# Kernel optimization log

Measured on AMD Instinct MI355X. Metric: run time of the kernel, lower is better.

The kernel has to match this reference:

```python
import jax, jax.numpy as jnp
import numpy as np

H = 128

def _gru_cell(x, h, w_ih, w_hh, b_ih, b_hh):
    # PyTorch GRUCell semantics; w_* are [3H, H], gate order r, z, n.
    gi = x @ w_ih.T + b_ih
    gh = h @ w_hh.T + b_hh
    ir, iz, in_ = jnp.split(gi, 3, axis=-1)
    hr, hz, hn = jnp.split(gh, 3, axis=-1)
    r = jax.nn.sigmoid(ir + hr)
    z = jax.nn.sigmoid(iz + hz)
    n = jnp.tanh(in_ + r * hn)
    return (1.0 - z) * n + z * h


def setup_inputs() -> dict:
    key = jax.random.key(0)
    ks = jax.random.split(key, 24)
    s = 0.05
    d = {}
    d["weapon_features"] = jax.random.normal(ks[0], (4, 8, 64, 4), jnp.float32)
    d["target_features"] = jax.random.normal(ks[1], (4, 8, 64, 4), jnp.float32)
    d["edge_features"] = jax.random.uniform(ks[2], (4, 8, 64, 64, 1), jnp.float32)
    # projections (torch Linear convention: weight [out, in])
    d["wp_w"] = jax.random.normal(ks[3], (H, 4), jnp.float32) * s
    d["wp_b"] = jnp.zeros((H,), jnp.float32)
    d["tp_w"] = jax.random.normal(ks[4], (H, 4), jnp.float32) * s
    d["tp_b"] = jnp.zeros((H,), jnp.float32)
    d["ep_w"] = jax.random.normal(ks[5], (H, 1), jnp.float32) * s
    d["ep_b"] = jnp.zeros((H,), jnp.float32)
    # message / edge-update linears [H, 3H]
    d["eu_w"] = jax.random.normal(ks[6], (H, 3 * H), jnp.float32) * s
    d["eu_b"] = jnp.zeros((H,), jnp.float32)
    d["wm_w"] = jax.random.normal(ks[7], (H, 3 * H), jnp.float32) * s
    d["wm_b"] = jnp.zeros((H,), jnp.float32)
    d["tm_w"] = jax.random.normal(ks[8], (H, 3 * H), jnp.float32) * s
    d["tm_b"] = jnp.zeros((H,), jnp.float32)
    # GRU cells
    d["gru_w_ih_w"] = jax.random.normal(ks[9], (3 * H, H), jnp.float32) * s
    d["gru_w_hh_w"] = jax.random.normal(ks[10], (3 * H, H), jnp.float32) * s
    d["gru_b_ih_w"] = jnp.zeros((3 * H,), jnp.float32)
    d["gru_b_hh_w"] = jnp.zeros((3 * H,), jnp.float32)
    d["gru_w_ih_t"] = jax.random.normal(ks[11], (3 * H, H), jnp.float32) * s
    d["gru_w_hh_t"] = jax.random.normal(ks[12], (3 * H, H), jnp.float32) * s
    d["gru_b_ih_t"] = jnp.zeros((3 * H,), jnp.float32)
    d["gru_b_hh_t"] = jnp.zeros((3 * H,), jnp.float32)
    return d


def reference(weapon_features, target_features, edge_features,
              wp_w, wp_b, tp_w, tp_b, ep_w, ep_b,
              eu_w, eu_b, wm_w, wm_b, tm_w, tm_b,
              gru_w_ih_w, gru_w_hh_w, gru_b_ih_w, gru_b_hh_w,
              gru_w_ih_t, gru_w_hh_t, gru_b_ih_t, gru_b_hh_t):
    B, P, W = weapon_features.shape[:3]
    T = target_features.shape[2]
    h = wp_w.shape[0]

    weapon_h = weapon_features @ wp_w.T + wp_b          # [B,P,W,H]
    target_h = target_features @ tp_w.T + tp_b          # [B,P,T,H]
    edge_h = edge_features @ ep_w.T + ep_b              # [B,P,W,T,H]

    # edge_update(cat([w_exp, t_exp, edge_h])) == sum of three slice-linears,
    # broadcast-added; avoids materializing the [B,P,W,T,3H] concat.
    ea, eb, ec = eu_w[:, :h], eu_w[:, h:2 * h], eu_w[:, 2 * h:]
    edge_pre = ((weapon_h @ ea.T)[:, :, :, None, :]
                + (target_h @ eb.T)[:, :, None, :, :]
                + edge_h @ ec.T + eu_b)
    edge_h_new = jnp.tanh(edge_pre)                     # [B,P,W,T,H]

    # weapon_msg(cat([w_exp, t_exp, edge_h_new])).sum(dim=3)
    wa, wb, wc = wm_w[:, :h], wm_w[:, h:2 * h], wm_w[:, 2 * h:]
    weapon_msgs = (T * (weapon_h @ wa.T)
                   + (target_h.sum(axis=2) @ wb.T)[:, :, None, :]
                   + edge_h_new.sum(axis=3) @ wc.T
                   + T * wm_b)                          # [B,P,W,H]

    # target_msg(cat([t_exp, w_exp, edge_h_new])).sum(dim=2)
    ta, tb, tc = tm_w[:, :h], tm_w[:, h:2 * h], tm_w[:, 2 * h:]
    target_msgs = (W * (target_h @ ta.T)
                   + (weapon_h.sum(axis=2) @ tb.T)[:, :, None, :]
                   + edge_h_new.sum(axis=2) @ tc.T
                   + W * tm_b)                          # [B,P,T,H]

    weapon_h_new = _gru_cell(weapon_msgs.reshape(-1, h), weapon_h.reshape(-1, h),
                             gru_w_ih_w, gru_w_hh_w, gru_b_ih_w, gru_b_hh_w)
    weapon_h_new = weapon_h_new.reshape(B, P, W, h)

    target_h_new = _gru_cell(target_msgs.reshape(-1, h), target_h.reshape(-1, h),
                             gru_w_ih_t, gru_w_hh_t, gru_b_ih_t, gru_b_hh_t)
    target_h_new = target_h_new.reshape(B, P, T, h)

    return weapon_h_new, target_h_new, edge_h_new
```

## Files before the change

### kernel.cpp

```cpp
#include <hip/hip_runtime.h>

#define DEV __device__ __forceinline__

constexpr int H  = 128;
constexpr int BP = 32;
constexpr int NR = 2048;

constexpr int WH_OFF    = 0;
constexpr int TH_OFF    = WH_OFF + NR*H;
constexpr int WHS_OFF   = TH_OFF + NR*H;
constexpr int THS_OFF   = WHS_OFF + BP*H;
constexpr int V1_OFF    = THS_OFF + BP*H;
constexpr int C0_OFF    = V1_OFF + H;
constexpr int WT1_OFF   = C0_OFF + H;
constexpr int WT2_OFF   = WT1_OFF + 128*640;
constexpr int WCT_OFF   = WT2_OFF + 128*640;
constexpr int TCT_OFF   = WCT_OFF + 128*128;
constexpr int WIHWT_OFF = TCT_OFF + 128*128;
constexpr int WIHTT_OFF = WIHWT_OFF + 128*384;
constexpr int WBT_OFF   = WIHTT_OFF + 128*384;
constexpr int TBT_OFF   = WBT_OFF + 128*128;
constexpr int OUT1_OFF  = TBT_OFF + 128*128;
constexpr int OUT2_OFF  = OUT1_OFF + NR*640;
constexpr int ESW_OFF   = OUT2_OFF + NR*640;
constexpr int ESTP_OFF  = ESW_OFF + NR*H;
constexpr int MSGW_OFF  = ESTP_OFF + 8*NR*H;
constexpr int MSGT_OFF  = MSGW_OFF + NR*H;
constexpr int GIW_OFF   = MSGT_OFF + NR*H;
constexpr int GIT_OFF   = GIW_OFF + NR*384;
constexpr int WBV_OFF   = GIT_OFF + NR*384;
constexpr int TBV_OFF   = WBV_OFF + BP*H;

DEV float fast_tanh(float x) {
  float e = __builtin_amdgcn_exp2f(x * 2.8853900817779268f);
  return fmaf(-2.0f, __builtin_amdgcn_rcpf(e + 1.0f), 1.0f);
}
DEV float fast_sigmoid(float x) {
  float e = __builtin_amdgcn_exp2f(x * -1.4426950408889634f);
  return __builtin_amdgcn_rcpf(1.0f + e);
}

__global__ __launch_bounds__(256) void ka_prep(
    const float* __restrict__ wf, const float* __restrict__ tf,
    const float* __restrict__ wp_w, const float* __restrict__ wp_b,
    const float* __restrict__ tp_w, const float* __restrict__ tp_b,
    const float* __restrict__ eu_w, const float* __restrict__ wm_w,
    const float* __restrict__ tm_w,
    const float* __restrict__ whh_w, const float* __restrict__ whh_t,
    const float* __restrict__ wih_w, const float* __restrict__ wih_t,
    const float* __restrict__ ep_w, const float* __restrict__ ep_b,
    const float* __restrict__ eu_b,
    float* __restrict__ ws)
{
  int bid = blockIdx.x, tid = threadIdx.x;
  if (bid < 2048) {
    int gid = bid*256 + tid;
    int m = gid >> 7;
    int j = gid & 127;
    int side = m >> 11;
    int n = m & 2047;
    const float* F  = side ? tf : wf;
    const float* Pw = side ? tp_w : wp_w;
    const float* Pb = side ? tp_b : wp_b;
    float4 x  = *(const float4*)&F[n*4];
    float4 wv = *(const float4*)&Pw[j*4];
    float v = x.x*wv.x + x.y*wv.y + x.z*wv.z + x.w*wv.w + Pb[j];
    ws[(side ? TH_OFF : WH_OFF) + n*H + j] = v;
  } else if (bid == 2048) {
    __shared__ float fs[2][32][4];
    {
      int side = tid >> 7, r = tid & 127;
      int bp = r >> 2, c = r & 3;
      const float* F = side ? tf : wf;
      float s = 0.f;
      #pragma unroll 8
      for (int w = 0; w < 64; ++w) s += F[bp*256 + w*4 + c];
      fs[side][bp][c] = s;
    }
    __syncthreads();
    {
      int side = tid >> 7, j = tid & 127;
      const float* Pw = side ? tp_w : wp_w;
      const float* Pb = side ? tp_b : wp_b;
      float4 wv = *(const float4*)&Pw[j*4];
      float pb = Pb[j] * 64.f;
      float* dst = ws + (side ? THS_OFF : WHS_OFF) + j;
      #pragma unroll 4
      for (int bp = 0; bp < 32; ++bp) {
        float4 f = *(const float4*)&fs[side][bp][0];
        dst[bp*128] = f.x*wv.x + f.y*wv.y + f.z*wv.z + f.w*wv.w + pb;
      }
    }
    if (tid < 128) {
      int j = tid;
      float s1 = 0.f, s0 = 0.f;
      for (int k = 0; k < 128; ++k) {
        float ec = eu_w[j*384 + 256 + k];
        s1 = fmaf(ec, ep_w[k], s1);
        s0 = fmaf(ec, ep_b[k], s0);
      }
      ws[V1_OFF + j] = s1;
      ws[C0_OFF + j] = s0 + eu_b[j];
    }
  } else {
    __shared__ float T[128*133];
    int tt = bid - 2049;
    const float* src; int rs = 384, co = 0, row0 = 0, dsto, ldd, j0;
    switch (tt) {
      case 0:  src=eu_w;  dsto=WT1_OFF; ldd=640; j0=0;   break;
      case 1:  src=wm_w;  dsto=WT1_OFF; ldd=640; j0=128; break;
      case 2: case 3: case 4:
        src=whh_w; rs=128; row0=(tt-2)*128; dsto=WT1_OFF; ldd=640; j0=256+(tt-2)*128; break;
      case 5:  src=eu_w;  co=128; dsto=WT2_OFF; ldd=640; j0=0; break;
      case 6:  src=tm_w;  dsto=WT2_OFF; ldd=640; j0=128; break;
      case 7: case 8: case 9:
        src=whh_t; rs=128; row0=(tt-7)*128; dsto=WT2_OFF; ldd=640; j0=256+(tt-7)*128; break;
      case 10: src=wm_w; co=256; dsto=WCT_OFF; ldd=128; j0=0; break;
      case 11: src=tm_w; co=256; dsto=TCT_OFF; ldd=128; j0=0; break;
      case 12: src=wm_w; co=128; dsto=WBT_OFF; ldd=128; j0=0; break;
      case 13: src=tm_w; co=128; dsto=TBT_OFF; ldd=128; j0=0; break;
      case 14: case 15: case 16:
        src=wih_w; rs=128; row0=(tt-14)*128; dsto=WIHWT_OFF; ldd=384; j0=(tt-14)*128; break;
      default:
        src=wih_t; rs=128; row0=(tt-17)*128; dsto=WIHTT_OFF; ldd=384; j0=(tt-17)*128; break;
    }
    #pragma unroll
    for (int q = 0; q < 16; ++q) {
      int idx = q*1024 + tid*4;
      int r = idx >> 7, c = idx & 127;
      float4 v = *(const float4*)&src[(row0 + r)*rs + co + c];
      float* t = &T[r*133 + c];
      t[0]=v.x; t[1]=v.y; t[2]=v.z; t[3]=v.w;
    }
    __syncthreads();
    float* dst = ws + dsto;
    #pragma unroll
    for (int q = 0; q < 64; ++q) {
      int idx = q*256 + tid;
      int k = idx >> 7, j = idx & 127;
      dst[k*ldd + j0 + j] = T[j*133 + k];
    }
  }
}

#define FMA4(A, s, Wv) do { A.x = fmaf(s, Wv.x, A.x); A.y = fmaf(s, Wv.y, A.y); \
                            A.z = fmaf(s, Wv.z, A.z); A.w = fmaf(s, Wv.w, A.w); } while (0)

DEV void stage_x32(float* Xs, const float* __restrict__ X, int row0, int tid) {
  const float* src = X + row0*128;
  #pragma unroll
  for (int q = 0; q < 4; ++q) {
    int idx = q*1024 + tid*4;
    *(float4*)&Xs[idx] = *(const float4*)&src[idx];
  }
}

DEV void stage_x64(float* Xs, const float* __restrict__ X, int row0, int tid) {
  const float* src = X + row0*128;
  #pragma unroll
  for (int q = 0; q < 8; ++q) {
    int idx = q*1024 + tid*4;
    *(float4*)&Xs[idx] = *(const float4*)&src[idx];
  }
}

DEV void stage_x_sum8(float* Xs, const float* __restrict__ base, int row0, int tid) {
  #pragma unroll
  for (int q = 0; q < 4; ++q) {
    int idx = q*1024 + tid*4;
    float4 s = *(const float4*)&base[row0*128 + idx];
    #pragma unroll
    for (int wt = 1; wt < 8; ++wt) {
      float4 v = *(const float4*)&base[wt*(NR*H) + row0*128 + idx];
      s.x += v.x; s.y += v.y; s.z += v.z; s.w += v.w;
    }
    *(float4*)&Xs[idx] = s;
  }
}

DEV void gemm_core32(const float* __restrict__ Wt, int ldw, int j0,
                     const float* Xs, float* Ws, int tid, float4 acc[4])
{
  const int tc = tid & 31, tr = tid >> 5;
  const int jj = tc*4, r0 = tr*4;
  #pragma unroll
  for (int i = 0; i < 4; ++i) acc[i] = make_float4(0.f, 0.f, 0.f, 0.f);
  for (int kc = 0; kc < 128; kc += 32) {
    __syncthreads();
    #pragma unroll
    for (int q = 0; q < 4; ++q) {
      int idx = q*1024 + tid*4;
      int kk = idx >> 7, j = idx & 127;
      *(float4*)&Ws[idx] = *(const float4*)&Wt[(kc+kk)*ldw + j0 + j];
    }
    __syncthreads();
    #pragma unroll
    for (int kk = 0; kk < 32; kk += 4) {
      float4 w0 = *(const float4*)&Ws[(kk+0)*128 + jj];
      float4 w1 = *(const float4*)&Ws[(kk+1)*128 + jj];
      float4 w2 = *(const float4*)&Ws[(kk+2)*128 + jj];
      float4 w3 = *(const float4*)&Ws[(kk+3)*128 + jj];
      #pragma unroll
      for (int rr = 0; rr < 4; ++rr) {
        float4 xq = *(const float4*)&Xs[(r0+rr)*128 + kc + kk];
        FMA4(acc[rr], xq.x, w0);
        FMA4(acc[rr], xq.y, w1);
        FMA4(acc[rr], xq.z, w2);
        FMA4(acc[rr], xq.w, w3);
      }
    }
  }
}

DEV void gemm_core64(const float* __restrict__ Wt, int ldw, int j0,
                     const float* Xs, float* Ws, int tid, float4 acc[8])
{
  const int tc = tid & 31, tr = tid >> 5;
  const int jj = tc*4, r0 = tr*8;
  #pragma unroll
  for (int i = 0; i < 8; ++i) acc[i] = make_float4(0.f, 0.f, 0.f, 0.f);
  for (int kc = 0; kc < 128; kc += 32) {
    __syncthreads();
    #pragma unroll
    for (int q = 0; q < 4; ++q) {
      int idx = q*1024 + tid*4;
      int kk = idx >> 7, j = idx & 127;
      *(float4*)&Ws[idx] = *(const float4*)&Wt[(kc+kk)*ldw + j0 + j];
    }
    __syncthreads();
    #pragma unroll
    for (int kk = 0; kk < 32; kk += 4) {
      float4 w0 = *(const float4*)&Ws[(kk+0)*128 + jj];
      float4 w1 = *(const float4*)&Ws[(kk+1)*128 + jj];
      float4 w2 = *(const float4*)&Ws[(kk+2)*128 + jj];
      float4 w3 = *(const float4*)&Ws[(kk+3)*128 + jj];
      #pragma unroll
      for (int rr = 0; rr < 8; ++rr) {
        float4 xq = *(const float4*)&Xs[(r0+rr)*128 + kc + kk];
        FMA4(acc[rr], xq.x, w0);
        FMA4(acc[rr], xq.y, w1);
        FMA4(acc[rr], xq.z, w2);
        FMA4(acc[rr], xq.w, w3);
      }
    }
  }
}

__global__ __launch_bounds__(256) void kb_gemm1(float* __restrict__ ws)
{
  __shared__ float Xs[64*128];
  __shared__ float Wsh[32*128];
  int bid = blockIdx.x, tid = threadIdx.x;
  const int tc = tid & 31, tr = tid >> 5;
  const int jj = tc*4;
  if (bid < 320) {
    int side = bid >= 160;
    int b2 = bid - (side ? 160 : 0);
    int rt = b2 & 31, ct = b2 >> 5;
    int row0 = rt*64;
    stage_x64(Xs, ws + (side ? TH_OFF : WH_OFF), row0, tid);
    float4 acc[8];
    gemm_core64(ws + (side ? WT2_OFF : WT1_OFF), 640, ct*128, Xs, Wsh, tid, acc);
    float* C = ws + (side ? OUT2_OFF : OUT1_OFF);
    const int r0 = tr*8;
    #pragma unroll
    for (int rr = 0; rr < 8; ++rr)
      *(float4*)&C[(row0+r0+rr)*640 + ct*128 + jj] = acc[rr];
  } else {
    int which = bid - 320;
    stage_x32(Xs, ws + (which ? WHS_OFF : THS_OFF), 0, tid);
    float4 acc[4];
    gemm_core32(ws + (which ? TBT_OFF : WBT_OFF), 128, 0, Xs, Wsh, tid, acc);
    float* C = ws + (which ? TBV_OFF : WBV_OFF);
    const int r0 = tr*4;
    #pragma unroll
    for (int rr = 0; rr < 4; ++rr)
      *(float4*)&C[(r0+rr)*128 + jj] = acc[rr];
  }
}

__global__ __launch_bounds__(256) void kc_edge(
    const float* __restrict__ ef, float* __restrict__ ws, float* __restrict__ out)
{
  __shared__ float Bs[64*128];
  __shared__ float e_lds[8*64];
  __shared__ float red[2][8][128];
  int bid = blockIdx.x, tid = threadIdx.x;
  int bp = bid >> 3, wq = bid & 7;
  int j = tid & 127, tsel = tid >> 7;
  float v1j = ws[V1_OFF + j], c0j = ws[C0_OFF + j];
  {
    const float* o2 = ws + OUT2_OFF + bp*64*640;
    #pragma unroll
    for (int q = 0; q < 8; ++q) {
      int idx = q*256 + tid;
      int t = idx >> 5, jq = (idx & 31)*4;
      *(float4*)&Bs[t*128 + jq] = *(const float4*)&o2[t*640 + jq];
    }
  }
  if (tid < 128) {
    int w = tid >> 4, t4 = (tid & 15)*4;
    *(float4*)&e_lds[w*64 + t4] = *(const float4*)&ef[bp*4096 + (wq*8 + w)*64 + t4];
  }
  float a_reg[8];
  #pragma unroll
  for (int w = 0; w < 8; ++w)
    a_reg[w] = ws[OUT1_OFF + (bp*64 + wq*8 + w)*640 + j];
  __syncthreads();
  float tsum[8] = {0,0,0,0,0,0,0,0};
  float* edst = out + 524288 + (bp*64 + wq*8)*8192 + j;
  float* pdst = ws + ESTP_OFF + wq*(NR*H) + bp*64*128 + j;
  for (int i = 0; i < 32; ++i) {
    int t = 2*i + tsel;
    float base = Bs[t*128 + j] + c0j;
    float wsum = 0.f;
    #pragma unroll
    for (int w = 0; w < 8; ++w) {
      float ev = e_lds[w*64 + t];
      float pre = a_reg[w] + fmaf(ev, v1j, base);
      float hv = fast_tanh(pre);
      __builtin_nontemporal_store(hv, &edst[w*8192 + t*128]);
      tsum[w] += hv;
      wsum += hv;
    }
    pdst[t*128] = wsum;
  }
  #pragma unroll
  for (int w = 0; w < 8; ++w) red[tsel][w][j] = tsum[w];
  __syncthreads();
  if (tsel == 0) {
    #pragma unroll
    for (int w = 0; w < 8; ++w)
      ws[ESW_OFF + (bp*64 + wq*8 + w)*128 + j] = red[0][w][j] + red[1][w][j];
  }
}

__global__ __launch_bounds__(256) void kd_gemm2(
    float* __restrict__ ws, const float* __restrict__ wm_b, const float* __restrict__ tm_b)
{
  __shared__ float Xs[32*128];
  __shared__ float Wsh[32*128];
  int bid = blockIdx.x, tid = threadIdx.x;
  int side = bid >> 6, rt = bid & 63;
  int row0 = rt*32;
  const int tc = tid & 31, tr = tid >> 5;
  const int jj = tc*4, r0 = tr*4;
  if (side == 0) stage_x32(Xs, ws + ESW_OFF, row0, tid);
  else           stage_x_sum8(Xs, ws + ESTP_OFF, row0, tid);
  float4 acc[4];
  gemm_core32(ws + (side ? TCT_OFF : WCT_OFF), 128, 0, Xs, Wsh, tid, acc);
  const float* OUTx = ws + (side ? OUT2_OFF : OUT1_OFF);
  const float* BV   = ws + (side ? TBV_OFF : WBV_OFF);
  const float* mb   = side ? tm_b : wm_b;
  float* MSG        = ws + (side ? MSGT_OFF : MSGW_OFF);
  float4 b4 = *(const float4*)&mb[jj];
  #pragma unroll
  for (int rr = 0; rr < 4; ++rr) {
    int n = row0 + r0 + rr;
    float4 wa4 = *(const float4*)&OUTx[n*640 + 128 + jj];
    float4 bv4 = *(const float4*)&BV[(n >> 6)*128 + jj];
    float4 r;
    r.x = acc[rr].x + 64.f*(wa4.x + b4.x) + bv4.x;
    r.y = acc[rr].y + 64.f*(wa4.y + b4.y) + bv4.y;
    r.z = acc[rr].z + 64.f*(wa4.z + b4.z) + bv4.z;
    r.w = acc[rr].w + 64.f*(wa4.w + b4.w) + bv4.w;
    *(float4*)&MSG[n*128 + jj] = r;
  }
}

__global__ __launch_bounds__(256) void ke_gemm3(float* __restrict__ ws)
{
  __shared__ float Xs[32*128];
  __shared__ float Wsh[32*128];
  int bid = blockIdx.x, tid = threadIdx.x;
  int side = bid >= 192;
  int b2 = bid - (side ? 192 : 0);
  int rt = b2 & 63, ct = b2 >> 6;
  int row0 = rt*32;
  const int tc = tid & 31, tr = tid >> 5;
  const int jj = tc*4, r0 = tr*4;
  stage_x32(Xs, ws + (side ? MSGT_OFF : MSGW_OFF), row0, tid);
  float4 acc[4];
  gemm_core32(ws + (side ? WIHTT_OFF : WIHWT_OFF), 384, ct*128, Xs, Wsh, tid, acc);
  float* C = ws + (side ? GIT_OFF : GIW_OFF);
  #pragma unroll
  for (int rr = 0; rr < 4; ++rr)
    *(float4*)&C[(row0+r0+rr)*384 + ct*128 + jj] = acc[rr];
}

__global__ __launch_bounds__(256) void kf_gru(
    const float* __restrict__ ws, float* __restrict__ out,
    const float* __restrict__ bih_w, const float* __restrict__ bhh_w,
    const float* __restrict__ bih_t, const float* __restrict__ bhh_t)
{
  int gid = blockIdx.x*256 + threadIdx.x;
  int jj = (gid & 31)*4;
  int n  = (gid >> 5) & 2047;
  int side = gid >> 16;
  const float* GI = ws + (side ? GIT_OFF : GIW_OFF) + n*384;
  const float* GH = ws + (side ? OUT2_OFF : OUT1_OFF) + n*640 + 256;
  const float* Hv = ws + (side ? TH_OFF : WH_OFF) + n*128;
  const float* bi = side ? bih_t : bih_w;
  const float* bh = side ? bhh_t : bhh_w;
  float4 gir = *(const float4*)&GI[jj];
  float4 giz = *(const float4*)&GI[128 + jj];
  float4 gin = *(const float4*)&GI[256 + jj];
  float4 ghr = *(const float4*)&GH[jj];
  float4 ghz = *(const float4*)&GH[128 + jj];
  float4 ghn = *(const float4*)&GH[256 + jj];
  float4 bir = *(const float4*)&bi[jj];
  float4 biz = *(const float4*)&bi[128 + jj];
  float4 bin = *(const float4*)&bi[256 + jj];
  float4 bhr = *(const float4*)&bh[jj];
  float4 bhz = *(const float4*)&bh[128 + jj];
  float4 bhn = *(const float4*)&bh[256 + jj];
  float4 h4  = *(const float4*)&Hv[jj];
  float4 o;
  #define GRU1(c) do { \
    float r = fast_sigmoid(gir.c + bir.c + ghr.c + bhr.c); \
    float z = fast_sigmoid(giz.c + biz.c + ghz.c + bhz.c); \
    float nn = fast_tanh(gin.c + bin.c + r*(ghn.c + bhn.c)); \
    o.c = (1.f - z)*nn + z*h4.c; } while (0)
  GRU1(x); GRU1(y); GRU1(z); GRU1(w);
  #undef GRU1
  __builtin_nontemporal_store(o.x, &out[side*262144 + n*128 + jj + 0]);
  __builtin_nontemporal_store(o.y, &out[side*262144 + n*128 + jj + 1]);
  __builtin_nontemporal_store(o.z, &out[side*262144 + n*128 + jj + 2]);
  __builtin_nontemporal_store(o.w, &out[side*262144 + n*128 + jj + 3]);
}

extern "C" void kernel_launch(void* const* d_in, const int* in_sizes, int n_in,
                              void* d_out, int out_size, void* d_ws, size_t ws_size,
                              hipStream_t stream)
{
  const float* wf    = (const float*)d_in[0];
  const float* tf    = (const float*)d_in[1];
  const float* ef    = (const float*)d_in[2];
  const float* wp_w  = (const float*)d_in[3];
  const float* wp_b  = (const float*)d_in[4];
  const float* tp_w  = (const float*)d_in[5];
  const float* tp_b  = (const float*)d_in[6];
  const float* ep_w  = (const float*)d_in[7];
  const float* ep_b  = (const float*)d_in[8];
  const float* eu_w  = (const float*)d_in[9];
  const float* eu_b  = (const float*)d_in[10];
  const float* wm_w  = (const float*)d_in[11];
  const float* wm_b  = (const float*)d_in[12];
  const float* tm_w  = (const float*)d_in[13];
  const float* tm_b  = (const float*)d_in[14];
  const float* wih_w = (const float*)d_in[15];
  const float* whh_w = (const float*)d_in[16];
  const float* bih_w = (const float*)d_in[17];
  const float* bhh_w = (const float*)d_in[18];
  const float* wih_t = (const float*)d_in[19];
  const float* whh_t = (const float*)d_in[20];
  const float* bih_t = (const float*)d_in[21];
  const float* bhh_t = (const float*)d_in[22];
  float* ws  = (float*)d_ws;
  float* out = (float*)d_out;

  hipLaunchKernelGGL(ka_prep, dim3(2069), dim3(256), 0, stream,
                     wf, tf, wp_w, wp_b, tp_w, tp_b, eu_w, wm_w, tm_w,
                     whh_w, whh_t, wih_w, wih_t, ep_w, ep_b, eu_b, ws);
  hipLaunchKernelGGL(kb_gemm1, dim3(322),  dim3(256), 0, stream, ws);
  hipLaunchKernelGGL(kc_edge,  dim3(256),  dim3(256), 0, stream, ef, ws, out);
  hipLaunchKernelGGL(kd_gemm2, dim3(128),  dim3(256), 0, stream, ws, wm_b, tm_b);
  hipLaunchKernelGGL(ke_gemm3, dim3(384),  dim3(256), 0, stream, ws);
  hipLaunchKernelGGL(kf_gru,   dim3(512),  dim3(256), 0, stream, ws, out,
                     bih_w, bhh_w, bih_t, bhh_t);
}
```

Baseline: 186.6 us.

## Fuse projections into GEMM1 and merge message, input-gate GEMM and GRU kernels

The node feature projections and per-batch sums move out of the prep kernel and are computed in shared memory inside the first GEMM. That GEMM also writes the projected hidden states for later use. The message GEMM, the GRU input GEMM and the GRU elementwise step are merged into one kernel working on 16-row tiles, so the MSG and GI intermediates never go through global memory. This cuts the launch count from six to four and removes several global round trips. In exchange, the fused kernel has smaller tiles and repeats the weight staging for each of the three gate column blocks.

```diff
diff --git a/kernel.cpp b/kernel.cpp
--- a/kernel.cpp
+++ b/kernel.cpp
@@ -8,9 +8,7 @@
 
 constexpr int WH_OFF    = 0;
 constexpr int TH_OFF    = WH_OFF + NR*H;
-constexpr int WHS_OFF   = TH_OFF + NR*H;
-constexpr int THS_OFF   = WHS_OFF + BP*H;
-constexpr int V1_OFF    = THS_OFF + BP*H;
+constexpr int V1_OFF    = TH_OFF + NR*H;
 constexpr int C0_OFF    = V1_OFF + H;
 constexpr int WT1_OFF   = C0_OFF + H;
 constexpr int WT2_OFF   = WT1_OFF + 128*640;
@@ -24,11 +22,7 @@
 constexpr int OUT2_OFF  = OUT1_OFF + NR*640;
 constexpr int ESW_OFF   = OUT2_OFF + NR*640;
 constexpr int ESTP_OFF  = ESW_OFF + NR*H;
-constexpr int MSGW_OFF  = ESTP_OFF + 8*NR*H;
-constexpr int MSGT_OFF  = MSGW_OFF + NR*H;
-constexpr int GIW_OFF   = MSGT_OFF + NR*H;
-constexpr int GIT_OFF   = GIW_OFF + NR*384;
-constexpr int WBV_OFF   = GIT_OFF + NR*384;
+constexpr int WBV_OFF   = ESTP_OFF + 8*NR*H;
 constexpr int TBV_OFF   = WBV_OFF + BP*H;
 
 DEV float fast_tanh(float x) {
@@ -40,10 +34,7 @@
   return __builtin_amdgcn_rcpf(1.0f + e);
 }
 
-__global__ __launch_bounds__(256) void ka_prep(
-    const float* __restrict__ wf, const float* __restrict__ tf,
-    const float* __restrict__ wp_w, const float* __restrict__ wp_b,
-    const float* __restrict__ tp_w, const float* __restrict__ tp_b,
+__global__ __launch_bounds__(256) void k0_prep(
     const float* __restrict__ eu_w, const float* __restrict__ wm_w,
     const float* __restrict__ tm_w,
     const float* __restrict__ whh_w, const float* __restrict__ whh_t,
@@ -52,139 +43,76 @@
     const float* __restrict__ eu_b,
     float* __restrict__ ws)
 {
-  int bid = blockIdx.x, tid = threadIdx.x;
-  if (bid < 2048) {
-    int gid = bid*256 + tid;
-    int m = gid >> 7;
-    int j = gid & 127;
-    int side = m >> 11;
-    int n = m & 2047;
-    const float* F  = side ? tf : wf;
-    const float* Pw = side ? tp_w : wp_w;
-    const float* Pb = side ? tp_b : wp_b;
-    float4 x  = *(const float4*)&F[n*4];
-    float4 wv = *(const float4*)&Pw[j*4];
-    float v = x.x*wv.x + x.y*wv.y + x.z*wv.z + x.w*wv.w + Pb[j];
-    ws[(side ? TH_OFF : WH_OFF) + n*H + j] = v;
-  } else if (bid == 2048) {
-    __shared__ float fs[2][32][4];
-    {
-      int side = tid >> 7, r = tid & 127;
-      int bp = r >> 2, c = r & 3;
-      const float* F = side ? tf : wf;
-      float s = 0.f;
+  __shared__ float T[128*133];
+  __shared__ float epl[128], ebl[128];
+  int tt = blockIdx.x, tid = threadIdx.x;
+  const float* src; int rs = 384, co = 0, row0 = 0, dsto = 0, ldd = 0, j0 = 0;
+  switch (tt) {
+    case 0:  src=eu_w;  dsto=WT1_OFF; ldd=640; j0=0;   break;
+    case 1:  src=wm_w;  dsto=WT1_OFF; ldd=640; j0=128; break;
+    case 2: case 3: case 4:
+      src=whh_w; rs=128; row0=(tt-2)*128; dsto=WT1_OFF; ldd=640; j0=256+(tt-2)*128; break;
+    case 5:  src=eu_w;  co=128; dsto=WT2_OFF; ldd=640; j0=0; break;
+    case 6:  src=tm_w;  dsto=WT2_OFF; ldd=640; j0=128; break;
+    case 7: case 8: case 9:
+      src=whh_t; rs=128; row0=(tt-7)*128; dsto=WT2_OFF; ldd=640; j0=256+(tt-7)*128; break;
+    case 10: src=wm_w; co=256; dsto=WCT_OFF; ldd=128; j0=0; break;
+    case 11: src=tm_w; co=256; dsto=TCT_OFF; ldd=128; j0=0; break;
+    case 12: src=wm_w; co=128; dsto=WBT_OFF; ldd=128; j0=0; break;
+    case 13: src=tm_w; co=128; dsto=TBT_OFF; ldd=128; j0=0; break;
+    case 14: case 15: case 16:
+      src=wih_w; rs=128; row0=(tt-14)*128; dsto=WIHWT_OFF; ldd=384; j0=(tt-14)*128; break;
+    case 17: case 18: case 19:
+      src=wih_t; rs=128; row0=(tt-17)*128; dsto=WIHTT_OFF; ldd=384; j0=(tt-17)*128; break;
+    default: src=eu_w; co=256; break;
+  }
+  #pragma unroll
+  for (int q = 0; q < 16; ++q) {
+    int idx = q*1024 + tid*4;
+    int r = idx >> 7, c = idx & 127;
+    float4 v = *(const float4*)&src[(row0 + r)*rs + co + c];
+    float* t = &T[r*133 + c];
+    t[0]=v.x; t[1]=v.y; t[2]=v.z; t[3]=v.w;
+  }
+  if (tt == 20 && tid >= 128) {
+    epl[tid-128] = ep_w[tid-128];
+    ebl[tid-128] = ep_b[tid-128];
+  }
+  __syncthreads();
+  if (tt == 20) {
+    if (tid < 128) {
+      float s1 = 0.f, s0 = 0.f;
       #pragma unroll 8
-      for (int w = 0; w < 64; ++w) s += F[bp*256 + w*4 + c];
-      fs[side][bp][c] = s;
-    }
-    __syncthreads();
-    {
-      int side = tid >> 7, j = tid & 127;
-      const float* Pw = side ? tp_w : wp_w;
-      const float* Pb = side ? tp_b : wp_b;
-      float4 wv = *(const float4*)&Pw[j*4];
-      float pb = Pb[j] * 64.f;
-      float* dst = ws + (side ? THS_OFF : WHS_OFF) + j;
-      #pragma unroll 4
-      for (int bp = 0; bp < 32; ++bp) {
-        float4 f = *(const float4*)&fs[side][bp][0];
-        dst[bp*128] = f.x*wv.x + f.y*wv.y + f.z*wv.z + f.w*wv.w + pb;
-      }
-    }
-    if (tid < 128) {
-      int j = tid;
-      float s1 = 0.f, s0 = 0.f;
       for (int k = 0; k < 128; ++k) {
-        float ec = eu_w[j*384 + 256 + k];
-        s1 = fmaf(ec, ep_w[k], s1);
-        s0 = fmaf(ec, ep_b[k], s0);
-      }
-      ws[V1_OFF + j] = s1;
-      ws[C0_OFF + j] = s0 + eu_b[j];
-    }
-  } else {
-    __shared__ float T[128*133];
-    int tt = bid - 2049;
-    const float* src; int rs = 384, co = 0, row0 = 0, dsto, ldd, j0;
-    switch (tt) {
-      case 0:  src=eu_w;  dsto=WT1_OFF; ldd=640; j0=0;   break;
-      case 1:  src=wm_w;  dsto=WT1_OFF; ldd=640; j0=128; break;
-      case 2: case 3: case 4:
-        src=whh_w; rs=128; row0=(tt-2)*128; dsto=WT1_OFF; ldd=640; j0=256+(tt-2)*128; break;
-      case 5:  src=eu_w;  co=128; dsto=WT2_OFF; ldd=640; j0=0; break;
-      case 6:  src=tm_w;  dsto=WT2_OFF; ldd=640; j0=128; break;
-      case 7: case 8: case 9:
-        src=whh_t; rs=128; row0=(tt-7)*128; dsto=WT2_OFF; ldd=640; j0=256+(tt-7)*128; break;
-      case 10: src=wm_w; co=256; dsto=WCT_OFF; ldd=128; j0=0; break;
-      case 11: src=tm_w; co=256; dsto=TCT_OFF; ldd=128; j0=0; break;
-      case 12: src=wm_w; co=128; dsto=WBT_OFF; ldd=128; j0=0; break;
-      case 13: src=tm_w; co=128; dsto=TBT_OFF; ldd=128; j0=0; break;
-      case 14: case 15: case 16:
-        src=wih_w; rs=128; row0=(tt-14)*128; dsto=WIHWT_OFF; ldd=384; j0=(tt-14)*128; break;
-      default:
-        src=wih_t; rs=128; row0=(tt-17)*128; dsto=WIHTT_OFF; ldd=384; j0=(tt-17)*128; break;
-    }
-    #pragma unroll
-    for (int q = 0; q < 16; ++q) {
-      int idx = q*1024 + tid*4;
-      int r = idx >> 7, c = idx & 127;
-      float4 v = *(const float4*)&src[(row0 + r)*rs + co + c];
-      float* t = &T[r*133 + c];
-      t[0]=v.x; t[1]=v.y; t[2]=v.z; t[3]=v.w;
-    }
-    __syncthreads();
-    float* dst = ws + dsto;
-    #pragma unroll
-    for (int q = 0; q < 64; ++q) {
-      int idx = q*256 + tid;
-      int k = idx >> 7, j = idx & 127;
-      dst[k*ldd + j0 + j] = T[j*133 + k];
-    }
+        float ec = T[tid*133 + k];
+        s1 = fmaf(ec, epl[k], s1);
+        s0 = fmaf(ec, ebl[k], s0);
+      }
+      ws[V1_OFF + tid] = s1;
+      ws[C0_OFF + tid] = s0 + eu_b[tid];
+    }
+    return;
+  }
+  float* dst = ws + dsto;
+  #pragma unroll
+  for (int q = 0; q < 64; ++q) {
+    int idx = q*256 + tid;
+    int k = idx >> 7, j = idx & 127;
+    dst[k*ldd + j0 + j] = T[j*133 + k];
   }
 }
 
 #define FMA4(A, s, Wv) do { A.x = fmaf(s, Wv.x, A.x); A.y = fmaf(s, Wv.y, A.y); \
                             A.z = fmaf(s, Wv.z, A.z); A.w = fmaf(s, Wv.w, A.w); } while (0)
 
-DEV void stage_x32(float* Xs, const float* __restrict__ X, int row0, int tid) {
-  const float* src = X + row0*128;
-  #pragma unroll
-  for (int q = 0; q < 4; ++q) {
-    int idx = q*1024 + tid*4;
-    *(float4*)&Xs[idx] = *(const float4*)&src[idx];
-  }
-}
-
-DEV void stage_x64(float* Xs, const float* __restrict__ X, int row0, int tid) {
-  const float* src = X + row0*128;
-  #pragma unroll
-  for (int q = 0; q < 8; ++q) {
-    int idx = q*1024 + tid*4;
-    *(float4*)&Xs[idx] = *(const float4*)&src[idx];
-  }
-}
-
-DEV void stage_x_sum8(float* Xs, const float* __restrict__ base, int row0, int tid) {
-  #pragma unroll
-  for (int q = 0; q < 4; ++q) {
-    int idx = q*1024 + tid*4;
-    float4 s = *(const float4*)&base[row0*128 + idx];
-    #pragma unroll
-    for (int wt = 1; wt < 8; ++wt) {
-      float4 v = *(const float4*)&base[wt*(NR*H) + row0*128 + idx];
-      s.x += v.x; s.y += v.y; s.z += v.z; s.w += v.w;
-    }
-    *(float4*)&Xs[idx] = s;
-  }
-}
-
-DEV void gemm_core32(const float* __restrict__ Wt, int ldw, int j0,
-                     const float* Xs, float* Ws, int tid, float4 acc[4])
+template<int RPT>
+DEV void gemm_coreN(const float* __restrict__ Wt, int ldw, int j0,
+                    const float* Xs, float* Ws, int tid, float4* acc)
 {
   const int tc = tid & 31, tr = tid >> 5;
-  const int jj = tc*4, r0 = tr*4;
-  #pragma unroll
-  for (int i = 0; i < 4; ++i) acc[i] = make_float4(0.f, 0.f, 0.f, 0.f);
+  const int jj = tc*4, r0 = tr*RPT;
+  #pragma unroll
+  for (int i = 0; i < RPT; ++i) acc[i] = make_float4(0.f, 0.f, 0.f, 0.f);
   for (int kc = 0; kc < 128; kc += 32) {
     __syncthreads();
     #pragma unroll
@@ -201,7 +129,7 @@
       float4 w2 = *(const float4*)&Ws[(kk+2)*128 + jj];
       float4 w3 = *(const float4*)&Ws[(kk+3)*128 + jj];
       #pragma unroll
-      for (int rr = 0; rr < 4; ++rr) {
+      for (int rr = 0; rr < RPT; ++rr) {
         float4 xq = *(const float4*)&Xs[(r0+rr)*128 + kc + kk];
         FMA4(acc[rr], xq.x, w0);
         FMA4(acc[rr], xq.y, w1);
@@ -212,44 +140,18 @@
   }
 }
 
-DEV void gemm_core64(const float* __restrict__ Wt, int ldw, int j0,
-                     const float* Xs, float* Ws, int tid, float4 acc[8])
-{
-  const int tc = tid & 31, tr = tid >> 5;
-  const int jj = tc*4, r0 = tr*8;
-  #pragma unroll
-  for (int i = 0; i < 8; ++i) acc[i] = make_float4(0.f, 0.f, 0.f, 0.f);
-  for (int kc = 0; kc < 128; kc += 32) {
-    __syncthreads();
-    #pragma unroll
-    for (int q = 0; q < 4; ++q) {
-      int idx = q*1024 + tid*4;
-      int kk = idx >> 7, j = idx & 127;
-      *(float4*)&Ws[idx] = *(const float4*)&Wt[(kc+kk)*ldw + j0 + j];
-    }
-    __syncthreads();
-    #pragma unroll
-    for (int kk = 0; kk < 32; kk += 4) {
-      float4 w0 = *(const float4*)&Ws[(kk+0)*128 + jj];
-      float4 w1 = *(const float4*)&Ws[(kk+1)*128 + jj];
-      float4 w2 = *(const float4*)&Ws[(kk+2)*128 + jj];
-      float4 w3 = *(const float4*)&Ws[(kk+3)*128 + jj];
-      #pragma unroll
-      for (int rr = 0; rr < 8; ++rr) {
-        float4 xq = *(const float4*)&Xs[(r0+rr)*128 + kc + kk];
-        FMA4(acc[rr], xq.x, w0);
-        FMA4(acc[rr], xq.y, w1);
-        FMA4(acc[rr], xq.z, w2);
-        FMA4(acc[rr], xq.w, w3);
-      }
-    }
-  }
-}
-
-__global__ __launch_bounds__(256) void kb_gemm1(float* __restrict__ ws)
+__global__ __launch_bounds__(256) void k1_gemm1(
+    const float* __restrict__ wf, const float* __restrict__ tf,
+    const float* __restrict__ wp_w, const float* __restrict__ wp_b,
+    const float* __restrict__ tp_w, const float* __restrict__ tp_b,
+    float* __restrict__ ws)
 {
   __shared__ float Xs[64*128];
   __shared__ float Wsh[32*128];
+  __shared__ float4 Fls[64];
+  __shared__ float4 Wls[128];
+  __shared__ float  Bls[128];
+  __shared__ float  fs[32][4];
   int bid = blockIdx.x, tid = threadIdx.x;
   const int tc = tid & 31, tr = tid >> 5;
   const int jj = tc*4;
@@ -258,19 +160,67 @@
     int b2 = bid - (side ? 160 : 0);
     int rt = b2 & 31, ct = b2 >> 5;
     int row0 = rt*64;
-    stage_x64(Xs, ws + (side ? TH_OFF : WH_OFF), row0, tid);
+    const float* F  = side ? tf : wf;
+    const float* Pw = side ? tp_w : wp_w;
+    const float* Pb = side ? tp_b : wp_b;
+    if (tid < 64)        Fls[tid]     = *(const float4*)&F[(row0 + tid)*4];
+    else if (tid < 192)  Wls[tid-64]  = *(const float4*)&Pw[(tid-64)*4];
+    else { int j = (tid-192)*2; Bls[j] = Pb[j]; Bls[j+1] = Pb[j+1]; }
+    __syncthreads();
+    {
+      int j = tid & 127, half = tid >> 7;
+      float4 wv = Wls[j]; float b = Bls[j];
+      #pragma unroll
+      for (int rr = 0; rr < 32; ++rr) {
+        int r = half*32 + rr;
+        float4 f = Fls[r];
+        Xs[r*128 + j] = f.x*wv.x + f.y*wv.y + f.z*wv.z + f.w*wv.w + b;
+      }
+    }
     float4 acc[8];
-    gemm_core64(ws + (side ? WT2_OFF : WT1_OFF), 640, ct*128, Xs, Wsh, tid, acc);
+    gemm_coreN<8>(ws + (side ? WT2_OFF : WT1_OFF), 640, ct*128, Xs, Wsh, tid, acc);
     float* C = ws + (side ? OUT2_OFF : OUT1_OFF);
     const int r0 = tr*8;
     #pragma unroll
     for (int rr = 0; rr < 8; ++rr)
       *(float4*)&C[(row0+r0+rr)*640 + ct*128 + jj] = acc[rr];
+    if (ct == 0) {
+      float* Hdst = ws + (side ? TH_OFF : WH_OFF) + row0*128;
+      #pragma unroll
+      for (int q = 0; q < 8; ++q) {
+        int idx = q*1024 + tid*4;
+        *(float4*)&Hdst[idx] = *(const float4*)&Xs[idx];
+      }
+    }
   } else {
     int which = bid - 320;
-    stage_x32(Xs, ws + (which ? WHS_OFF : THS_OFF), 0, tid);
+    const float* F  = which ? wf : tf;
+    const float* Pw = which ? wp_w : tp_w;
+    const float* Pb = which ? wp_b : tp_b;
+    if (tid < 128) {
+      int bp = tid >> 2, c = tid & 3;
+      float s = 0.f;
+      #pragma unroll 8
+      for (int w = 0; w < 64; ++w) s += F[bp*256 + w*4 + c];
+      fs[bp][c] = s;
+    } else {
+      int j = tid - 128;
+      Wls[j] = *(const float4*)&Pw[j*4];
+      Bls[j] = Pb[j];
+    }
+    __syncthreads();
+    {
+      int j = tid & 127, half = tid >> 7;
+      float4 wv = Wls[j]; float b = Bls[j]*64.f;
+      #pragma unroll
+      for (int rr = 0; rr < 16; ++rr) {
+        int r = half*16 + rr;
+        float4 f = *(const float4*)&fs[r][0];
+        Xs[r*128 + j] = f.x*wv.x + f.y*wv.y + f.z*wv.z + f.w*wv.w + b;
+      }
+    }
     float4 acc[4];
-    gemm_core32(ws + (which ? TBT_OFF : WBT_OFF), 128, 0, Xs, Wsh, tid, acc);
+    gemm_coreN<4>(ws + (which ? TBT_OFF : WBT_OFF), 128, 0, Xs, Wsh, tid, acc);
     float* C = ws + (which ? TBV_OFF : WBV_OFF);
     const int r0 = tr*4;
     #pragma unroll
@@ -279,7 +229,7 @@
   }
 }
 
-__global__ __launch_bounds__(256) void kc_edge(
+__global__ __launch_bounds__(256) void k2_edge(
     const float* __restrict__ ef, float* __restrict__ ws, float* __restrict__ out)
 {
   __shared__ float Bs[64*128];
@@ -335,98 +285,92 @@
   }
 }
 
-__global__ __launch_bounds__(256) void kd_gemm2(
-    float* __restrict__ ws, const float* __restrict__ wm_b, const float* __restrict__ tm_b)
-{
-  __shared__ float Xs[32*128];
+__global__ __launch_bounds__(256) void k3_fused(
+    float* __restrict__ ws, float* __restrict__ out,
+    const float* __restrict__ wm_b, const float* __restrict__ tm_b,
+    const float* __restrict__ bih_w, const float* __restrict__ bhh_w,
+    const float* __restrict__ bih_t, const float* __restrict__ bhh_t)
+{
+  __shared__ float Xin[16*128];
+  __shared__ float Xm[16*128];
   __shared__ float Wsh[32*128];
   int bid = blockIdx.x, tid = threadIdx.x;
-  int side = bid >> 6, rt = bid & 63;
-  int row0 = rt*32;
+  int side = bid >> 7, rt = bid & 127, row0 = rt*16;
   const int tc = tid & 31, tr = tid >> 5;
-  const int jj = tc*4, r0 = tr*4;
-  if (side == 0) stage_x32(Xs, ws + ESW_OFF, row0, tid);
-  else           stage_x_sum8(Xs, ws + ESTP_OFF, row0, tid);
-  float4 acc[4];
-  gemm_core32(ws + (side ? TCT_OFF : WCT_OFF), 128, 0, Xs, Wsh, tid, acc);
+  const int jj = tc*4;
+  #pragma unroll
+  for (int q = 0; q < 2; ++q) {
+    int idx = q*1024 + tid*4;
+    float4 v;
+    if (side == 0) {
+      v = *(const float4*)&ws[ESW_OFF + row0*128 + idx];
+    } else {
+      v = *(const float4*)&ws[ESTP_OFF + row0*128 + idx];
+      #pragma unroll
+      for (int wt = 1; wt < 8; ++wt) {
+        float4 u = *(const float4*)&ws[ESTP_OFF + wt*(NR*H) + row0*128 + idx];
+        v.x += u.x; v.y += u.y; v.z += u.z; v.w += u.w;
+      }
+    }
+    *(float4*)&Xin[idx] = v;
+  }
+  float4 accm[2];
+  gemm_coreN<2>(ws + (side ? TCT_OFF : WCT_OFF), 128, 0, Xin, Wsh, tid, accm);
   const float* OUTx = ws + (side ? OUT2_OFF : OUT1_OFF);
-  const float* BV   = ws + (side ? TBV_OFF : WBV_OFF);
-  const float* mb   = side ? tm_b : wm_b;
-  float* MSG        = ws + (side ? MSGT_OFF : MSGW_OFF);
-  float4 b4 = *(const float4*)&mb[jj];
-  #pragma unroll
-  for (int rr = 0; rr < 4; ++rr) {
-    int n = row0 + r0 + rr;
-    float4 wa4 = *(const float4*)&OUTx[n*640 + 128 + jj];
-    float4 bv4 = *(const float4*)&BV[(n >> 6)*128 + jj];
-    float4 r;
-    r.x = acc[rr].x + 64.f*(wa4.x + b4.x) + bv4.x;
-    r.y = acc[rr].y + 64.f*(wa4.y + b4.y) + bv4.y;
-    r.z = acc[rr].z + 64.f*(wa4.z + b4.z) + bv4.z;
-    r.w = acc[rr].w + 64.f*(wa4.w + b4.w) + bv4.w;
-    *(float4*)&MSG[n*128 + jj] = r;
-  }
-}
-
-__global__ __launch_bounds__(256) void ke_gemm3(float* __restrict__ ws)
-{
-  __shared__ float Xs[32*128];
-  __shared__ float Wsh[32*128];
-  int bid = blockIdx.x, tid = threadIdx.x;
-  int side = bid >= 192;
-  int b2 = bid - (side ? 192 : 0);
-  int rt = b2 & 63, ct = b2 >> 6;
-  int row0 = rt*32;
-  const int tc = tid & 31, tr = tid >> 5;
-  const int jj = tc*4, r0 = tr*4;
-  stage_x32(Xs, ws + (side ? MSGT_OFF : MSGW_OFF), row0, tid);
-  float4 acc[4];
-  gemm_core32(ws + (side ? WIHTT_OFF : WIHWT_OFF), 384, ct*128, Xs, Wsh, tid, acc);
-  float* C = ws + (side ? GIT_OFF : GIW_OFF);
-  #pragma unroll
-  for (int rr = 0; rr < 4; ++rr)
-    *(float4*)&C[(row0+r0+rr)*384 + ct*128 + jj] = acc[rr];
-}
-
-__global__ __launch_bounds__(256) void kf_gru(
-    const float* __restrict__ ws, float* __restrict__ out,
-    const float* __restrict__ bih_w, const float* __restrict__ bhh_w,
-    const float* __restrict__ bih_t, const float* __restrict__ bhh_t)
-{
-  int gid = blockIdx.x*256 + threadIdx.x;
-  int jj = (gid & 31)*4;
-  int n  = (gid >> 5) & 2047;
-  int side = gid >> 16;
-  const float* GI = ws + (side ? GIT_OFF : GIW_OFF) + n*384;
-  const float* GH = ws + (side ? OUT2_OFF : OUT1_OFF) + n*640 + 256;
-  const float* Hv = ws + (side ? TH_OFF : WH_OFF) + n*128;
-  const float* bi = side ? bih_t : bih_w;
-  const float* bh = side ? bhh_t : bhh_w;
-  float4 gir = *(const float4*)&GI[jj];
-  float4 giz = *(const float4*)&GI[128 + jj];
-  float4 gin = *(const float4*)&GI[256 + jj];
-  float4 ghr = *(const float4*)&GH[jj];
-  float4 ghz = *(const float4*)&GH[128 + jj];
-  float4 ghn = *(const float4*)&GH[256 + jj];
-  float4 bir = *(const float4*)&bi[jj];
-  float4 biz = *(const float4*)&bi[128 + jj];
-  float4 bin = *(const float4*)&bi[256 + jj];
-  float4 bhr = *(const float4*)&bh[jj];
-  float4 bhz = *(const float4*)&bh[128 + jj];
-  float4 bhn = *(const float4*)&bh[256 + jj];
-  float4 h4  = *(const float4*)&Hv[jj];
-  float4 o;
-  #define GRU1(c) do { \
-    float r = fast_sigmoid(gir.c + bir.c + ghr.c + bhr.c); \
-    float z = fast_sigmoid(giz.c + biz.c + ghz.c + bhz.c); \
-    float nn = fast_tanh(gin.c + bin.c + r*(ghn.c + bhn.c)); \
-    o.c = (1.f - z)*nn + z*h4.c; } while (0)
-  GRU1(x); GRU1(y); GRU1(z); GRU1(w);
-  #undef GRU1
-  __builtin_nontemporal_store(o.x, &out[side*262144 + n*128 + jj + 0]);
-  __builtin_nontemporal_store(o.y, &out[side*262144 + n*128 + jj + 1]);
-  __builtin_nontemporal_store(o.z, &out[side*262144 + n*128 + jj + 2]);
-  __builtin_nontemporal_store(o.w, &out[side*262144 + n*128 + jj + 3]);
+  {
+    const float* BV = ws + (side ? TBV_OFF : WBV_OFF);
+    const float* mb = side ? tm_b : wm_b;
+    float4 b4 = *(const float4*)&mb[jj];
+    #pragma unroll
+    for (int rr = 0; rr < 2; ++rr) {
+      int r = tr*2 + rr, n = row0 + r;
+      float4 wa4 = *(const float4*)&OUTx[n*640 + 128 + jj];
+      float4 bv4 = *(const float4*)&BV[(n >> 6)*128 + jj];
+      float4 m;
+      m.x = accm[rr].x + 64.f*(wa4.x + b4.x) + bv4.x;
+      m.y = accm[rr].y + 64.f*(wa4.y + b4.y) + bv4.y;
+      m.z = accm[rr].z + 64.f*(wa4.z + b4.z) + bv4.z;
+      m.w = accm[rr].w + 64.f*(wa4.w + b4.w) + bv4.w;
+      *(float4*)&Xm[r*128 + jj] = m;
+    }
+  }
+  const float* WIH = ws + (side ? WIHTT_OFF : WIHWT_OFF);
+  float4 ar[2], az[2], an[2];
+  gemm_coreN<2>(WIH, 384, 0,   Xm, Wsh, tid, ar);
+  gemm_coreN<2>(WIH, 384, 128, Xm, Wsh, tid, az);
+  gemm_coreN<2>(WIH, 384, 256, Xm, Wsh, tid, an);
+  {
+    const float* Hsrc = ws + (side ? TH_OFF : WH_OFF);
+    const float* bi = side ? bih_t : bih_w;
+    const float* bh = side ? bhh_t : bhh_w;
+    float4 bir = *(const float4*)&bi[jj];
+    float4 biz = *(const float4*)&bi[128 + jj];
+    float4 bin = *(const float4*)&bi[256 + jj];
+    float4 bhr = *(const float4*)&bh[jj];
+    float4 bhz = *(const float4*)&bh[128 + jj];
+    float4 bhn = *(const float4*)&bh[256 + jj];
+    #pragma unroll
+    for (int rr = 0; rr < 2; ++rr) {
+      int n = row0 + tr*2 + rr;
+      float4 ghr = *(const float4*)&OUTx[n*640 + 256 + jj];
+      float4 ghz = *(const float4*)&OUTx[n*640 + 384 + jj];
+      float4 ghn = *(const float4*)&OUTx[n*640 + 512 + jj];
+      float4 h4  = *(const float4*)&Hsrc[n*128 + jj];
+      float4 o;
+      #define GRU1(c) do { \
+        float r = fast_sigmoid(ar[rr].c + bir.c + ghr.c + bhr.c); \
+        float z = fast_sigmoid(az[rr].c + biz.c + ghz.c + bhz.c); \
+        float nn = fast_tanh(an[rr].c + bin.c + r*(ghn.c + bhn.c)); \
+        o.c = (1.f - z)*nn + z*h4.c; } while (0)
+      GRU1(x); GRU1(y); GRU1(z); GRU1(w);
+      #undef GRU1
+      float* op = &out[side*262144 + n*128 + jj];
+      __builtin_nontemporal_store(o.x, op + 0);
+      __builtin_nontemporal_store(o.y, op + 1);
+      __builtin_nontemporal_store(o.z, op + 2);
+      __builtin_nontemporal_store(o.w, op + 3);
+    }
+  }
 }
 
 extern "C" void kernel_launch(void* const* d_in, const int* in_sizes, int n_in,
@@ -459,13 +403,11 @@
   float* ws  = (float*)d_ws;
   float* out = (float*)d_out;
 
-  hipLaunchKernelGGL(ka_prep, dim3(2069), dim3(256), 0, stream,
-                     wf, tf, wp_w, wp_b, tp_w, tp_b, eu_w, wm_w, tm_w,
-                     whh_w, whh_t, wih_w, wih_t, ep_w, ep_b, eu_b, ws);
-  hipLaunchKernelGGL(kb_gemm1, dim3(322),  dim3(256), 0, stream, ws);
-  hipLaunchKernelGGL(kc_edge,  dim3(256),  dim3(256), 0, stream, ef, ws, out);
-  hipLaunchKernelGGL(kd_gemm2, dim3(128),  dim3(256), 0, stream, ws, wm_b, tm_b);
-  hipLaunchKernelGGL(ke_gemm3, dim3(384),  dim3(256), 0, stream, ws);
-  hipLaunchKernelGGL(kf_gru,   dim3(512),  dim3(256), 0, stream, ws, out,
-                     bih_w, bhh_w, bih_t, bhh_t);
-}
+  hipLaunchKernelGGL(k0_prep, dim3(21), dim3(256), 0, stream,
+                     eu_w, wm_w, tm_w, whh_w, whh_t, wih_w, wih_t, ep_w, ep_b, eu_b, ws);
+  hipLaunchKernelGGL(k1_gemm1, dim3(322), dim3(256), 0, stream,
+                     wf, tf, wp_w, wp_b, tp_w, tp_b, ws);
+  hipLaunchKernelGGL(k2_edge,  dim3(256), dim3(256), 0, stream, ef, ws, out);
+  hipLaunchKernelGGL(k3_fused, dim3(256), dim3(256), 0, stream, ws, out,
+                     wm_b, tm_b, bih_w, bhh_w, bih_t, bhh_t);
+}
```

Result: faster. 176.9 us (-5.2%).
